# Kernel tuning notes

Measured on AMD Instinct MI355X. Metric: run time of the kernel, lower is better.

## Reference

```python
import jax, jax.numpy as jnp
import numpy as np

N, D_IN, H, C, K = 4096, 512, 256, 64, 10
SCAD_A = 3.7
LAM_HAT = 0.9
LAM_BASE = 1.0 / LAM_HAT - 1.0  # global skip strength ~0.1111
EPS = 1e-6
DIST_EPS = 1e-8  # smoothing inside sqrt of pairwise distance


def setup_inputs() -> dict:
    key = jax.random.key(0)
    ks = jax.random.split(key, 5)
    A = jax.random.uniform(ks[0], (N, N), dtype=jnp.float32)  # dense weighted adjacency
    X = jax.random.normal(ks[1], (N, D_IN), dtype=jnp.float32)
    W1 = jax.random.normal(ks[2], (D_IN, H), dtype=jnp.float32) * 0.05
    b1 = jnp.zeros((H,), dtype=jnp.float32)
    W2 = jax.random.normal(ks[3], (H, C), dtype=jnp.float32) * 0.05
    b2 = jnp.zeros((C,), dtype=jnp.float32)
    lam_init = 6.0 / SCAD_A  # gamma_init / scad_a, 'uniform' strategy
    log_lams = jnp.full((K,), float(np.log(lam_init)), dtype=jnp.float32)
    # raw_alpha s.t. softplus(raw_alpha)+0.5 == alpha_init == 1.0
    raw_alpha = jnp.asarray(float(np.log(np.exp(0.5) - 1.0)), dtype=jnp.float32)
    return {"A": A, "X": X, "W1": W1, "b1": b1, "W2": W2, "b2": b2,
            "log_lams": log_lams, "raw_alpha": raw_alpha}


def _scad_weight(y, lam_k):
    # IRLS weight rho'(y)/(2y) for SCAD: lam for y<=lam; (a*lam-y)/(a-1) on (lam, a*lam]; 0 beyond.
    # y is sqrt(Z + DIST_EPS) >= 1e-4; cap at 1.0 as the y->0 numerical cap.
    mid = jnp.clip(SCAD_A * lam_k - y, 0.0, None) / (SCAD_A - 1.0)
    rho_prime = jnp.where(y <= lam_k, lam_k, mid)
    return jnp.minimum(rho_prime / (2.0 * y), 1.0)


def reference(A, X, W1, b1, W2, b2, log_lams, raw_alpha):
    # --- MLP (eval mode, dropout off) ---
    F0 = jnp.maximum(X @ W1 + b1, 0.0) @ W2 + b2  # [N, C]
    # --- per-node confidence lambda ('protect_uncertain', normalized) ---
    alpha = jax.nn.softplus(raw_alpha) + 0.5
    conf = jnp.clip(jax.nn.softmax(F0, axis=-1).max(axis=-1), EPS, 1.0 - EPS)
    raw_lam = LAM_BASE * jnp.clip(1.0 - conf, EPS, None) ** alpha
    lam_node = raw_lam * (LAM_BASE / jnp.clip(raw_lam.mean(), EPS, None))
    lam_node = jnp.clip(lam_node, EPS, None)  # [N]
    # --- graph normalization ---
    n = A.shape[0]
    A = A + jnp.eye(n, dtype=A.dtype)          # add_loops
    deg = A.sum(axis=-1)                       # [N]
    d_sq = jnp.sqrt(deg)[:, None]              # [N,1]
    A_tilde = A / (d_sq * d_sq.T)              # sym_norm: D^-1/2 A D^-1/2
    # --- K QN-IRLS steps ---
    F = F0
    for k in range(K):
        lam_k = jnp.exp(log_lams[k])
        Y = F / d_sq                                               # [N,C]
        sq = jnp.sum(Y * Y, axis=-1)                               # [N]
        Z = jnp.clip(sq[:, None] + sq[None, :] - 2.0 * (Y @ Y.T), 0.0, None)
        y = jnp.sqrt(Z + DIST_EPS)                                 # pairwise dist [N,N]
        Wt = _scad_weight(y, lam_k) * A_tilde                      # reweighted adjacency
        q = Wt.sum(axis=-1)                                        # [N]
        F = (Wt @ F + lam_node[:, None] * F0) / (q + lam_node)[:, None]
    return F
```

## Files before the change

### kernel.cpp

```cpp
#include <hip/hip_runtime.h>
#include <math.h>


#define NN 4096
#define DIN 512
#define HID 256
#define CD 64
#define NSPLIT 32
#define JT_PER 2

static constexpr float SCAD_Af   = 3.7f;
static constexpr float EPSf      = 1e-6f;
static constexpr float DIST_EPSf = 1e-8f;
#define LAM_BASEF ((float)(1.0 / 0.9 - 1.0))

typedef __attribute__((ext_vector_type(8))) short bf16x8;
typedef __attribute__((ext_vector_type(4))) float f32x4;

#define MFMA16(a, b, c) __builtin_amdgcn_mfma_f32_16x16x32_bf16((a), (b), (c), 0, 0, 0)

__device__ inline unsigned short f2bf(float f) {
    unsigned u = __float_as_uint(f);
    u += 0x7FFFu + ((u >> 16) & 1u);
    return (unsigned short)(u >> 16);
}
__device__ inline float bf2f(unsigned short h) {
    return __uint_as_float(((unsigned)h) << 16);
}

__device__ inline int yperm_off(int row, int c) {
    const int tile = row >> 6, ct = (row >> 4) & 3, m = row & 15;
    return (tile * 8 + ct * 2 + (c >> 5)) * 512 + ((c >> 3) & 3) * 128 + m * 8 + (c & 7);
}
__device__ inline int fperm_off(int row, int c) {
    const int tile = row >> 6;
    return (tile * 8 + (c >> 4) * 2 + ((row >> 5) & 1)) * 512
         + (((row >> 3) & 3) * 16 + (c & 15)) * 8 + (row & 7);
}

__global__ __launch_bounds__(256) void k_gemm1(const float* __restrict__ X,
    const float* __restrict__ W1, const float* __restrict__ b1,
    float* __restrict__ Hid)
{
    __shared__ float Xs[16][68];
    __shared__ float Ws[16][68];
    const int tid = threadIdx.x;
    const int tx = tid & 15, ty = tid >> 4;
    const int M0 = blockIdx.x * 64, N0 = blockIdx.y * 64;
    float acc[4][4] = {};
    for (int k0 = 0; k0 < DIN; k0 += 16) {
        __syncthreads();
        {
            const int kk = tid & 15, mm = tid >> 4;
            #pragma unroll
            for (int r = 0; r < 4; ++r)
                Xs[kk][mm + 16*r] = X[(size_t)(M0 + mm + 16*r) * DIN + k0 + kk];
            const int n = tid & 63, kw = tid >> 6;
            #pragma unroll
            for (int r = 0; r < 4; ++r)
                Ws[kw + 4*r][n] = W1[(size_t)(k0 + kw + 4*r) * HID + N0 + n];
        }
        __syncthreads();
        #pragma unroll
        for (int kk = 0; kk < 16; ++kk) {
            const float4 av = *(const float4*)&Xs[kk][4*ty];
            const float4 bv = *(const float4*)&Ws[kk][4*tx];
            const float a[4] = {av.x, av.y, av.z, av.w};
            const float b[4] = {bv.x, bv.y, bv.z, bv.w};
            #pragma unroll
            for (int i = 0; i < 4; ++i)
                #pragma unroll
                for (int j = 0; j < 4; ++j)
                    acc[i][j] = fmaf(a[i], b[j], acc[i][j]);
        }
    }
    #pragma unroll
    for (int i = 0; i < 4; ++i)
        #pragma unroll
        for (int j = 0; j < 4; ++j) {
            const int gn = N0 + 4*tx + j;
            const float v = acc[i][j] + b1[gn];
            Hid[(size_t)(M0 + 4*ty + i) * HID + gn] = fmaxf(v, 0.0f);
        }
}

__global__ __launch_bounds__(256) void k_gemm2(const float* __restrict__ Hd,
    const float* __restrict__ W2, const float* __restrict__ b2,
    float* __restrict__ F0)
{
    __shared__ float Hs[16][68];
    __shared__ float Ws[16][68];
    const int tid = threadIdx.x;
    const int tx = tid & 15, ty = tid >> 4;
    const int M0 = blockIdx.x * 64;
    float acc[4][4] = {};
    for (int k0 = 0; k0 < HID; k0 += 16) {
        __syncthreads();
        {
            const int kk = tid & 15, mm = tid >> 4;
            #pragma unroll
            for (int r = 0; r < 4; ++r)
                Hs[kk][mm + 16*r] = Hd[(size_t)(M0 + mm + 16*r) * HID + k0 + kk];
            const int n = tid & 63, kw = tid >> 6;
            #pragma unroll
            for (int r = 0; r < 4; ++r)
                Ws[kw + 4*r][n] = W2[(size_t)(k0 + kw + 4*r) * CD + n];
        }
        __syncthreads();
        #pragma unroll
        for (int kk = 0; kk < 16; ++kk) {
            const float4 av = *(const float4*)&Hs[kk][4*ty];
            const float4 bv = *(const float4*)&Ws[kk][4*tx];
            const float a[4] = {av.x, av.y, av.z, av.w};
            const float b[4] = {bv.x, bv.y, bv.z, bv.w};
            #pragma unroll
            for (int i = 0; i < 4; ++i)
                #pragma unroll
                for (int j = 0; j < 4; ++j)
                    acc[i][j] = fmaf(a[i], b[j], acc[i][j]);
        }
    }
    #pragma unroll
    for (int i = 0; i < 4; ++i)
        #pragma unroll
        for (int j = 0; j < 4; ++j) {
            const int gn = 4*tx + j;
            F0[(size_t)(M0 + 4*ty + i) * CD + gn] = acc[i][j] + b2[gn];
        }
}

__global__ __launch_bounds__(256) void k_conf(const float* __restrict__ F0,
    const float* __restrict__ raw_alpha, float* __restrict__ raw_lam)
{
    const int lane = threadIdx.x & 63;
    const int row  = blockIdx.x * 4 + (threadIdx.x >> 6);
    const float alpha = log1pf(expf(raw_alpha[0])) + 0.5f;
    const float f = F0[(size_t)row * CD + lane];
    float m = f;
    #pragma unroll
    for (int o = 32; o > 0; o >>= 1) m = fmaxf(m, __shfl_xor(m, o, 64));
    float e = expf(f - m);
    #pragma unroll
    for (int o = 32; o > 0; o >>= 1) e += __shfl_xor(e, o, 64);
    float conf = 1.0f / e;
    conf = fminf(fmaxf(conf, EPSf), 1.0f - EPSf);
    const float rl = LAM_BASEF * powf(fmaxf(1.0f - conf, EPSf), alpha);
    if (lane == 0) raw_lam[row] = rl;
}

__global__ __launch_bounds__(256) void k_lam(const float* __restrict__ raw_lam,
    float* __restrict__ lam_node)
{
    __shared__ float red[256];
    float s = 0.0f;
    for (int i = threadIdx.x; i < NN; i += 256) s += raw_lam[i];
    red[threadIdx.x] = s;
    __syncthreads();
    for (int o = 128; o > 0; o >>= 1) {
        if (threadIdx.x < o) red[threadIdx.x] += red[threadIdx.x + o];
        __syncthreads();
    }
    const float mean  = red[0] * (1.0f / NN);
    const float scale = LAM_BASEF / fmaxf(mean, EPSf);
    for (int i = threadIdx.x; i < NN; i += 256)
        lam_node[i] = fmaxf(raw_lam[i] * scale, EPSf);
}

__global__ __launch_bounds__(256) void k_deg(const float* __restrict__ A,
    float* __restrict__ u)
{
    __shared__ float red[256];
    const int i = blockIdx.x;
    float s = 0.0f;
    for (int j = threadIdx.x; j < NN; j += 256) s += A[(size_t)i * NN + j];
    red[threadIdx.x] = s;
    __syncthreads();
    for (int o = 128; o > 0; o >>= 1) {
        if (threadIdx.x < o) red[threadIdx.x] += red[threadIdx.x + o];
        __syncthreads();
    }
    if (threadIdx.x == 0) u[i] = 1.0f / sqrtf(red[0] + 1.0f);
}

__global__ __launch_bounds__(256) void k_castA(const float* __restrict__ A,
    unsigned short* __restrict__ Abf)
{
    __shared__ unsigned short t_lds[4096];
    const int ti = blockIdx.x >> 6, tj = blockIdx.x & 63;
    const int t = threadIdx.x;
    const int r = t >> 2, cq = t & 3;
    const size_t arow = (size_t)(ti * 64 + r) * NN + tj * 64 + cq * 16;
    #pragma unroll
    for (int q = 0; q < 4; ++q) {
        const float4 v = *(const float4*)(A + arow + 4 * q);
        const float vv[4] = {v.x, v.y, v.z, v.w};
        #pragma unroll
        for (int e = 0; e < 4; ++e) {
            const int cc = 4 * q + e;
            const int pos = ((r >> 2) * 16 + cc) * 16 + cq * 4 + (r & 3);
            t_lds[pos] = f2bf(vv[e]);
        }
    }
    __syncthreads();
    const uint4* src = (const uint4*)&t_lds[t * 16];
    uint4* dst = (uint4*)(Abf + (size_t)blockIdx.x * 4096 + t * 16);
    dst[0] = src[0];
    dst[1] = src[1];
}

__global__ __launch_bounds__(256) void k_prep(const float* __restrict__ F,
    const float* __restrict__ u, unsigned short* __restrict__ Yph,
    unsigned short* __restrict__ Ypl, unsigned short* __restrict__ Fp,
    float2* __restrict__ squ)
{
    const int lane = threadIdx.x & 63;
    const int row  = blockIdx.x * 4 + (threadIdx.x >> 6);
    const float ui = u[row];
    const float f  = F[(size_t)row * CD + lane];
    const float yv = f * ui;
    const unsigned short h = f2bf(yv);
    const int yo = yperm_off(row, lane);
    Yph[yo] = h;
    Ypl[yo] = f2bf(yv - bf2f(h));
    Fp[fperm_off(row, lane)] = f2bf(f);
    float s2 = yv * yv;
    #pragma unroll
    for (int o = 32; o > 0; o >>= 1) s2 += __shfl_xor(s2, o, 64);
    if (lane == 0) squ[row] = make_float2(s2, 0.5f * ui);
}

template<bool ABF>
__global__ __launch_bounds__(256, 4) void k_fused(
    const float* __restrict__ A, const unsigned short* __restrict__ Abf,
    const unsigned short* __restrict__ Yph, const unsigned short* __restrict__ Ypl,
    const unsigned short* __restrict__ Fp, const float2* __restrict__ squ,
    const float* __restrict__ log_lams, const int k,
    float* __restrict__ partF, float* __restrict__ partQ)
{
    __shared__ __align__(16) unsigned short w_lds[4][16][72];
    const int tid = threadIdx.x, lane = tid & 63, wid = tid >> 6;
    const int m = lane & 15, b = lane >> 4;
    const int I0 = blockIdx.x * 64, js = blockIdx.y;

    const float lam   = __expf(log_lams[k]);
    const float invA1 = 1.0f / (SCAD_Af - 1.0f);
    const float c1    = SCAD_Af * lam * invA1;

    const size_t ybase = ((size_t)blockIdx.x * 8 + wid * 2) * 512 + (size_t)lane * 8;
    const bf16x8 yiH0 = *(const bf16x8*)(Yph + ybase);
    const bf16x8 yiH1 = *(const bf16x8*)(Yph + ybase + 512);
    const bf16x8 yiL0 = *(const bf16x8*)(Ypl + ybase);
    const bf16x8 yiL1 = *(const bf16x8*)(Ypl + ybase + 512);

    float sqi_r[4];
    #pragma unroll
    for (int reg = 0; reg < 4; ++reg)
        sqi_r[reg] = squ[I0 + 16*wid + 4*b + reg].x;

    f32x4 FV[4];
    #pragma unroll
    for (int ct = 0; ct < 4; ++ct) FV[ct] = (f32x4){0.f, 0.f, 0.f, 0.f};
    float qa[4] = {0.f, 0.f, 0.f, 0.f};

    const size_t afrag_off = (size_t)(64*wid + 16*b + m) * 16;
    bf16x8 aC0, aC1, aN0, aN1;
    if constexpr (ABF) {
        const size_t tb = ((size_t)blockIdx.x * 64 + (size_t)(js * JT_PER)) * 4096 + afrag_off;
        aC0 = *(const bf16x8*)(Abf + tb);
        aC1 = *(const bf16x8*)(Abf + tb + 8);
    }

    for (int jt = 0; jt < JT_PER; ++jt) {
        const int J0 = js * (64 * JT_PER) + jt * 64;
        const int Jt = J0 >> 6;

        if constexpr (ABF) {
            if (jt + 1 < JT_PER) {
                const size_t tb = ((size_t)blockIdx.x * 64 + (size_t)(js * JT_PER + jt + 1)) * 4096 + afrag_off;
                aN0 = *(const bf16x8*)(Abf + tb);
                aN1 = *(const bf16x8*)(Abf + tb + 8);
            }
        }

        float sqj[4], ujh[4];
        #pragma unroll
        for (int ct = 0; ct < 4; ++ct) {
            const float2 s = squ[J0 + 16*ct + m];
            sqj[ct] = s.x; ujh[ct] = s.y;
        }

        f32x4 g[4];
        #pragma unroll
        for (int ct = 0; ct < 4; ++ct) {
            const size_t jb = ((size_t)Jt * 8 + ct * 2) * 512 + (size_t)lane * 8;
            const bf16x8 bh0 = *(const bf16x8*)(Yph + jb);
            const bf16x8 bh1 = *(const bf16x8*)(Yph + jb + 512);
            const bf16x8 bl0 = *(const bf16x8*)(Ypl + jb);
            const bf16x8 bl1 = *(const bf16x8*)(Ypl + jb + 512);
            f32x4 acc = (f32x4){0.f, 0.f, 0.f, 0.f};
            acc = MFMA16(yiH0, bh0, acc);
            acc = MFMA16(yiH1, bh1, acc);
            acc = MFMA16(yiH0, bl0, acc);
            acc = MFMA16(yiH1, bl1, acc);
            acc = MFMA16(yiL0, bh0, acc);
            acc = MFMA16(yiL1, bh1, acc);
            g[ct] = acc;
        }

        float av[4][4];
        if constexpr (ABF) {
            #pragma unroll
            for (int reg = 0; reg < 4; ++reg) {
                av[reg][0] = bf2f((unsigned short)aC0[reg]);
                av[reg][1] = bf2f((unsigned short)aC0[4 + reg]);
                av[reg][2] = bf2f((unsigned short)aC1[reg]);
                av[reg][3] = bf2f((unsigned short)aC1[4 + reg]);
            }
        } else {
            #pragma unroll
            for (int reg = 0; reg < 4; ++reg) {
                const size_t arb = (size_t)(I0 + 16*wid + 4*b + reg) * NN + J0 + m;
                #pragma unroll
                for (int ct = 0; ct < 4; ++ct)
                    av[reg][ct] = A[arb + 16*ct];
            }
        }

        const bool diag = (J0 == I0);

        #pragma unroll
        for (int ct = 0; ct < 4; ++ct) {
            #pragma unroll
            for (int reg = 0; reg < 4; ++reg) {
                const float Z   = fmaf(-2.0f, g[ct][reg], sqi_r[reg] + sqj[ct]);
                const float Zp  = fmaxf(Z, 0.0f) + DIST_EPSf;
                const float rsq = __builtin_amdgcn_rsqf(Zp);
                const float y   = Zp * rsq;
                const float t1  = fmaf(-invA1, y, c1);
                const float rho = __builtin_amdgcn_fmed3f(t1, 0.0f, lam);
                const float wv  = fminf(rho * rsq, 2.0f);
                float aij = av[reg][ct];
                if (diag && ct == wid && m == 4*b + reg) aij += 1.0f;
                const float t = wv * aij * ujh[ct];
                qa[reg] += t;
                w_lds[wid][4*b + reg][m + 16*ct] = f2bf(t);
            }
        }

        #pragma unroll
        for (int ks = 0; ks < 2; ++ks) {
            const bf16x8 wf = *(const bf16x8*)&w_lds[wid][m][8*b + 32*ks];
            #pragma unroll
            for (int ct = 0; ct < 4; ++ct) {
                const bf16x8 ff = *(const bf16x8*)(Fp +
                    ((size_t)Jt * 8 + ct * 2 + ks) * 512 + (size_t)lane * 8);
                FV[ct] = MFMA16(wf, ff, FV[ct]);
            }
        }

        if constexpr (ABF) { aC0 = aN0; aC1 = aN1; }
    }

    const size_t base = (size_t)js * NN + I0 + 16*wid;
    #pragma unroll
    for (int ct = 0; ct < 4; ++ct)
        #pragma unroll
        for (int reg = 0; reg < 4; ++reg)
            partF[(base + 4*b + reg) * CD + m + 16*ct] = FV[ct][reg];

    #pragma unroll
    for (int reg = 0; reg < 4; ++reg) {
        float q = qa[reg];
        q += __shfl_xor(q, 1, 64);
        q += __shfl_xor(q, 2, 64);
        q += __shfl_xor(q, 4, 64);
        q += __shfl_xor(q, 8, 64);
        if (m == 0) partQ[base + 4*b + reg] = q;
    }
}

__global__ __launch_bounds__(256) void k_combine(
    const float* __restrict__ partF, const float* __restrict__ partQ,
    const float* __restrict__ F0, const float* __restrict__ lam_node,
    const float* __restrict__ u, float* __restrict__ Fout,
    unsigned short* __restrict__ Yph, unsigned short* __restrict__ Ypl,
    unsigned short* __restrict__ Fp, float2* __restrict__ squ)
{
    const int lane = threadIdx.x & 63;
    const int row  = blockIdx.x * 4 + (threadIdx.x >> 6);
    float acc = 0.0f, q = 0.0f;
    #pragma unroll
    for (int s = 0; s < NSPLIT; ++s) {
        acc += partF[((size_t)s * NN + row) * CD + lane];
        q   += partQ[(size_t)s * NN + row];
    }
    const float ui = u[row];
    const float ln = lam_node[row];
    const float f0 = F0[(size_t)row * CD + lane];
    const float fn = (acc * ui + ln * f0) / (q * ui + ln);
    Fout[(size_t)row * CD + lane] = fn;
    const float yv = fn * ui;
    const unsigned short h = f2bf(yv);
    const int yo = yperm_off(row, lane);
    Yph[yo] = h;
    Ypl[yo] = f2bf(yv - bf2f(h));
    Fp[fperm_off(row, lane)] = f2bf(fn);
    float s2 = yv * yv;
    #pragma unroll
    for (int o = 32; o > 0; o >>= 1) s2 += __shfl_xor(s2, o, 64);
    if (lane == 0) squ[row] = make_float2(s2, 0.5f * ui);
}

extern "C" void kernel_launch(void* const* d_in, const int* in_sizes, int n_in,
                              void* d_out, int out_size, void* d_ws, size_t ws_size,
                              hipStream_t stream)
{
    const float* A         = (const float*)d_in[0];
    const float* X         = (const float*)d_in[1];
    const float* W1        = (const float*)d_in[2];
    const float* b1        = (const float*)d_in[3];
    const float* W2        = (const float*)d_in[4];
    const float* b2        = (const float*)d_in[5];
    const float* log_lams  = (const float*)d_in[6];
    const float* raw_alpha = (const float*)d_in[7];
    float* out = (float*)d_out;

    char* p = (char*)d_ws;
    auto alloc = [&](size_t bytes) -> char* {
        char* r = p;
        p += (bytes + 255) & ~(size_t)255;
        return r;
    };
    float* Hid      = (float*)alloc((size_t)NN * HID * 4);
    float* F0       = (float*)alloc((size_t)NN * CD * 4);
    float* raw_lam  = (float*)alloc((size_t)NN * 4);
    float* lam_node = (float*)alloc((size_t)NN * 4);
    float* uvec     = (float*)alloc((size_t)NN * 4);
    float2* squ     = (float2*)alloc((size_t)NN * 8);
    float* Fbuf     = (float*)alloc((size_t)NN * CD * 4);
    unsigned short* Yph = (unsigned short*)alloc((size_t)NN * CD * 2);
    unsigned short* Ypl = (unsigned short*)alloc((size_t)NN * CD * 2);
    unsigned short* Fp  = (unsigned short*)alloc((size_t)NN * CD * 2);
    float* partF    = (float*)alloc((size_t)NSPLIT * NN * CD * 4);
    float* partQ    = (float*)alloc((size_t)NSPLIT * NN * 4);
    const size_t base_used = (size_t)(p - (char*)d_ws);
    const size_t abf_bytes = (size_t)NN * NN * 2;
    const bool use_abf = (ws_size >= base_used + abf_bytes + 4096);
    unsigned short* Abf = use_abf ? (unsigned short*)alloc(abf_bytes) : (unsigned short*)nullptr;

    k_gemm1<<<dim3(64, 4), 256, 0, stream>>>(X, W1, b1, Hid);
    k_gemm2<<<dim3(64),    256, 0, stream>>>(Hid, W2, b2, F0);
    k_conf <<<dim3(1024),  256, 0, stream>>>(F0, raw_alpha, raw_lam);
    k_lam  <<<dim3(1),     256, 0, stream>>>(raw_lam, lam_node);
    k_deg  <<<dim3(4096),  256, 0, stream>>>(A, uvec);
    k_prep <<<dim3(1024),  256, 0, stream>>>(F0, uvec, Yph, Ypl, Fp, squ);
    if (use_abf)
        k_castA<<<dim3(4096), 256, 0, stream>>>(A, Abf);

    for (int k = 0; k < 10; ++k) {
        float* Fout = (k == 9) ? out : Fbuf;
        if (use_abf)
            k_fused<true><<<dim3(64, NSPLIT), 256, 0, stream>>>(A, Abf, Yph, Ypl, Fp,
                squ, log_lams, k, partF, partQ);
        else
            k_fused<false><<<dim3(64, NSPLIT), 256, 0, stream>>>(A, Abf, Yph, Ypl, Fp,
                squ, log_lams, k, partF, partQ);
        k_combine<<<dim3(1024), 256, 0, stream>>>(partF, partQ, F0, lam_node, uvec,
                                                  Fout, Yph, Ypl, Fp, squ);
    }
}
```

Measured before the change: 551.0 us.

## Fuse degree sum into A cast and store split partials as fp16

The degree reduction now happens inside the A-to-bf16 cast kernel, using per-block row sums and atomics, so A is read once instead of twice. The per-split partial F sums are written as packed fp16 in a wave-native layout, which halves the partial-sum traffic between the fused kernel and the combine kernel. In exchange, partial sums lose precision to fp16 and could overflow or round. The degree now comes from atomic float accumulation, so its summation order is no longer fixed.

```diff
diff --git a/kernel.cpp b/kernel.cpp
--- a/kernel.cpp
+++ b/kernel.cpp
@@ -1,4 +1,5 @@
 #include <hip/hip_runtime.h>
+#include <hip/hip_fp16.h>
 #include <math.h>
 
 
@@ -182,18 +183,21 @@
     if (threadIdx.x == 0) u[i] = 1.0f / sqrtf(red[0] + 1.0f);
 }
 
-__global__ __launch_bounds__(256) void k_castA(const float* __restrict__ A,
-    unsigned short* __restrict__ Abf)
+__global__ __launch_bounds__(256) void k_castA_deg(const float* __restrict__ A,
+    unsigned short* __restrict__ Abf, float* __restrict__ deg)
 {
     __shared__ unsigned short t_lds[4096];
+    __shared__ float rsum[64][4];
     const int ti = blockIdx.x >> 6, tj = blockIdx.x & 63;
     const int t = threadIdx.x;
     const int r = t >> 2, cq = t & 3;
     const size_t arow = (size_t)(ti * 64 + r) * NN + tj * 64 + cq * 16;
+    float s = 0.0f;
     #pragma unroll
     for (int q = 0; q < 4; ++q) {
         const float4 v = *(const float4*)(A + arow + 4 * q);
         const float vv[4] = {v.x, v.y, v.z, v.w};
+        s += vv[0] + vv[1] + vv[2] + vv[3];
         #pragma unroll
         for (int e = 0; e < 4; ++e) {
             const int cc = 4 * q + e;
@@ -201,11 +205,23 @@
             t_lds[pos] = f2bf(vv[e]);
         }
     }
+    rsum[r][cq] = s;
     __syncthreads();
     const uint4* src = (const uint4*)&t_lds[t * 16];
     uint4* dst = (uint4*)(Abf + (size_t)blockIdx.x * 4096 + t * 16);
     dst[0] = src[0];
     dst[1] = src[1];
+    if (t < 64) {
+        const float d = rsum[t][0] + rsum[t][1] + rsum[t][2] + rsum[t][3];
+        atomicAdd(&deg[ti * 64 + t], d);
+    }
+}
+
+__global__ __launch_bounds__(256) void k_u(const float* __restrict__ deg,
+    float* __restrict__ u)
+{
+    const int i = blockIdx.x * 256 + threadIdx.x;
+    u[i] = 1.0f / sqrtf(deg[i] + 1.0f);
 }
 
 __global__ __launch_bounds__(256) void k_prep(const float* __restrict__ F,
@@ -235,7 +251,7 @@
     const unsigned short* __restrict__ Yph, const unsigned short* __restrict__ Ypl,
     const unsigned short* __restrict__ Fp, const float2* __restrict__ squ,
     const float* __restrict__ log_lams, const int k,
-    float* __restrict__ partF, float* __restrict__ partQ)
+    unsigned* __restrict__ partH, float* __restrict__ partQ)
 {
     __shared__ __align__(16) unsigned short w_lds[4][16][72];
     const int tid = threadIdx.x, lane = tid & 63, wid = tid >> 6;
@@ -361,13 +377,16 @@
         if constexpr (ABF) { aC0 = aN0; aC1 = aN1; }
     }
 
-    const size_t base = (size_t)js * NN + I0 + 16*wid;
+    const size_t wb = ((((size_t)js * 64 + blockIdx.x) * 4 + wid) * 8) * 64 + lane;
     #pragma unroll
     for (int ct = 0; ct < 4; ++ct)
         #pragma unroll
-        for (int reg = 0; reg < 4; ++reg)
-            partF[(base + 4*b + reg) * CD + m + 16*ct] = FV[ct][reg];
-
+        for (int h = 0; h < 2; ++h) {
+            const __half2 pk = __floats2half2_rn(FV[ct][2*h], FV[ct][2*h + 1]);
+            partH[wb + (size_t)(ct * 2 + h) * 64] = *(const unsigned*)&pk;
+        }
+
+    const size_t qbase = (size_t)js * NN + I0 + 16*wid;
     #pragma unroll
     for (int reg = 0; reg < 4; ++reg) {
         float q = qa[reg];
@@ -375,12 +394,12 @@
         q += __shfl_xor(q, 2, 64);
         q += __shfl_xor(q, 4, 64);
         q += __shfl_xor(q, 8, 64);
-        if (m == 0) partQ[base + 4*b + reg] = q;
+        if (m == 0) partQ[qbase + 4*b + reg] = q;
     }
 }
 
 __global__ __launch_bounds__(256) void k_combine(
-    const float* __restrict__ partF, const float* __restrict__ partQ,
+    const unsigned* __restrict__ partH, const float* __restrict__ partQ,
     const float* __restrict__ F0, const float* __restrict__ lam_node,
     const float* __restrict__ u, float* __restrict__ Fout,
     unsigned short* __restrict__ Yph, unsigned short* __restrict__ Ypl,
@@ -388,10 +407,18 @@
 {
     const int lane = threadIdx.x & 63;
     const int row  = blockIdx.x * 4 + (threadIdx.x >> 6);
+
+    const int bi = row >> 6, wid = (row >> 4) & 3, bq = (row >> 2) & 3, reg = row & 3;
+    const int ct = lane >> 4, m = lane & 15;
+    const int hh = reg >> 1, p = reg & 1;
+    const size_t boff = (((size_t)bi * 4 + wid) * 8 + ct * 2 + hh) * 64 + bq * 16 + m;
+
     float acc = 0.0f, q = 0.0f;
     #pragma unroll
     for (int s = 0; s < NSPLIT; ++s) {
-        acc += partF[((size_t)s * NN + row) * CD + lane];
+        const unsigned v = partH[(size_t)s * (64 * 4 * 8 * 64) + boff];
+        const __half2 hv = *(const __half2*)&v;
+        acc += p ? __high2float(hv) : __low2float(hv);
         q   += partQ[(size_t)s * NN + row];
     }
     const float ui = u[row];
@@ -436,12 +463,13 @@
     float* raw_lam  = (float*)alloc((size_t)NN * 4);
     float* lam_node = (float*)alloc((size_t)NN * 4);
     float* uvec     = (float*)alloc((size_t)NN * 4);
+    float* degacc   = (float*)alloc((size_t)NN * 4);
     float2* squ     = (float2*)alloc((size_t)NN * 8);
     float* Fbuf     = (float*)alloc((size_t)NN * CD * 4);
     unsigned short* Yph = (unsigned short*)alloc((size_t)NN * CD * 2);
     unsigned short* Ypl = (unsigned short*)alloc((size_t)NN * CD * 2);
     unsigned short* Fp  = (unsigned short*)alloc((size_t)NN * CD * 2);
-    float* partF    = (float*)alloc((size_t)NSPLIT * NN * CD * 4);
+    unsigned* partH = (unsigned*)alloc((size_t)NSPLIT * NN * CD * 2);
     float* partQ    = (float*)alloc((size_t)NSPLIT * NN * 4);
     const size_t base_used = (size_t)(p - (char*)d_ws);
     const size_t abf_bytes = (size_t)NN * NN * 2;
@@ -452,20 +480,24 @@
     k_gemm2<<<dim3(64),    256, 0, stream>>>(Hid, W2, b2, F0);
     k_conf <<<dim3(1024),  256, 0, stream>>>(F0, raw_alpha, raw_lam);
     k_lam  <<<dim3(1),     256, 0, stream>>>(raw_lam, lam_node);
-    k_deg  <<<dim3(4096),  256, 0, stream>>>(A, uvec);
+    if (use_abf) {
+        hipMemsetAsync(degacc, 0, (size_t)NN * 4, stream);
+        k_castA_deg<<<dim3(4096), 256, 0, stream>>>(A, Abf, degacc);
+        k_u<<<dim3(16), 256, 0, stream>>>(degacc, uvec);
+    } else {
+        k_deg<<<dim3(4096), 256, 0, stream>>>(A, uvec);
+    }
     k_prep <<<dim3(1024),  256, 0, stream>>>(F0, uvec, Yph, Ypl, Fp, squ);
-    if (use_abf)
-        k_castA<<<dim3(4096), 256, 0, stream>>>(A, Abf);
 
     for (int k = 0; k < 10; ++k) {
         float* Fout = (k == 9) ? out : Fbuf;
         if (use_abf)
             k_fused<true><<<dim3(64, NSPLIT), 256, 0, stream>>>(A, Abf, Yph, Ypl, Fp,
-                squ, log_lams, k, partF, partQ);
+                squ, log_lams, k, partH, partQ);
         else
             k_fused<false><<<dim3(64, NSPLIT), 256, 0, stream>>>(A, Abf, Yph, Ypl, Fp,
-                squ, log_lams, k, partF, partQ);
-        k_combine<<<dim3(1024), 256, 0, stream>>>(partF, partQ, F0, lam_node, uvec,
+                squ, log_lams, k, partH, partQ);
+        k_combine<<<dim3(1024), 256, 0, stream>>>(partH, partQ, F0, lam_node, uvec,
                                                   Fout, Yph, Ypl, Fp, squ);
     }
 }
```

After: 528.4 us. 1.04x faster.
